# Optimization experiments

Measured on AMD Instinct MI355X. Metric: run time of the kernel, lower is better.

Reference implementation:

```python
import jax, jax.numpy as jnp
import numpy as np

K = 1024
D = 64
BETA = 0.25
EPS = 1e-10


def setup_inputs() -> dict:
    key = jax.random.key(0)
    k1, k2 = jax.random.split(key)
    z = jax.random.normal(k1, (64, D, 32, 32), dtype=jnp.float32)
    # embedding.weight.data.uniform_(-1/K, 1/K)
    emb = jax.random.uniform(k2, (K, D), dtype=jnp.float32,
                             minval=-1.0 / K, maxval=1.0 / K)
    return {"z": z, "emb": emb}


def reference(z, emb):
    sg = jax.lax.stop_gradient
    B, C, H, W = z.shape  # C == D
    zp = jnp.transpose(z, (0, 2, 3, 1))            # [B,H,W,D]
    zf = zp.reshape(-1, C)                          # [N,D]
    # squared-euclidean distances via matmul (cdist expansion)
    d = (jnp.sum(zf ** 2, axis=1, keepdims=True)
         + jnp.sum(emb ** 2, axis=1)
         - 2.0 * jnp.matmul(zf, emb.T))             # [N,K]
    idx = jnp.argmin(d, axis=1)                     # [N] int
    z_q = emb[idx].reshape(zp.shape)                # gather == one-hot matmul
    loss = (jnp.mean((sg(z_q) - zp) ** 2)
            + BETA * jnp.mean((z_q - sg(zp)) ** 2))
    # straight-through estimator
    z_q_st = zp + sg(z_q - zp)
    # codebook usage perplexity
    n = zf.shape[0]
    e_mean = jnp.zeros((K,), dtype=zf.dtype).at[idx].add(1.0) / n
    perplexity = jnp.exp(-jnp.sum(e_mean * jnp.log(e_mean + EPS)))
    z_q_out = jnp.transpose(z_q_st, (0, 3, 1, 2))   # back to [B,D,H,W]
    return (loss, z_q_out, perplexity, idx.reshape(B, H, W))
```

## Files before the change

### kernel.cpp

```cpp
#include <hip/hip_runtime.h>

#define NVEC 65536
#define KC   1024
#define DD   64
#define NTILE 64
#define KW   256
#define KU   32

#define OUT_ZQ   1
#define OUT_PPL  4194305
#define OUT_IDX  4194306

#define WS_KEYS  0
#define WS_HIST  524288
#define WS_SUMSQ 528384
#define WS_SE    528392
#define WS_EMBT  532488

__global__ __launch_bounds__(256) void prep_kernel(const float* __restrict__ emb,
                                                   float* __restrict__ se,
                                                   float* __restrict__ embT) {
    __shared__ float tile[64][65];
    const int tid = threadIdx.x;
    const int k0  = blockIdx.x * 64;

    {
        const int r = tid >> 2, q = tid & 3;
        const float* row = emb + (size_t)(k0 + r) * 64 + q * 16;
        #pragma unroll
        for (int i = 0; i < 4; ++i) {
            float4 v = *(const float4*)(row + i * 4);
            tile[r][q * 16 + i * 4 + 0] = v.x;
            tile[r][q * 16 + i * 4 + 1] = v.y;
            tile[r][q * 16 + i * 4 + 2] = v.z;
            tile[r][q * 16 + i * 4 + 3] = v.w;
        }
    }
    __syncthreads();

    if (tid < 64) {
        float r[8];
        #pragma unroll
        for (int c = 0; c < 64; ++c) {
            float v = tile[tid][c];
            float s = __fmul_rn(v, v);
            if (c < 8) r[c] = s;
            else       r[c & 7] = __fadd_rn(r[c & 7], s);
        }
        se[k0 + tid] = __fadd_rn(
            __fadd_rn(__fadd_rn(r[0], r[1]), __fadd_rn(r[2], r[3])),
            __fadd_rn(__fadd_rn(r[4], r[5]), __fadd_rn(r[6], r[7])));
    }

    const int kl = tid & 63, cg = tid >> 6;
    #pragma unroll
    for (int i = 0; i < 16; ++i) {
        int c = cg * 16 + i;
        embT[(size_t)c * KC + k0 + kl] = tile[kl][c];
    }
}

__global__ __launch_bounds__(256)
void dist_kernel(const float* __restrict__ z,
                 const float* __restrict__ embT,
                 const float* __restrict__ se,
                 unsigned long long* __restrict__ keys) {
    __shared__ float zt[64][64];
    __shared__ float lds_sz[64];
    __shared__ unsigned long long red[64];

    const int tid  = threadIdx.x;
    const int lane = tid & 63;
    const int w    = tid >> 6;
    const int n0   = blockIdx.x * NTILE;
    const int b    = n0 >> 10;
    const int hw0  = n0 & 1023;

    {
        const float* zbase = z + (size_t)b * 65536 + hw0;
        #pragma unroll
        for (int j = 0; j < 4; ++j) {
            int idx = tid + j * 256;
            int c   = idx >> 4;
            int nl4 = (idx & 15) * 4;
            *(float4*)&zt[c][nl4] = *(const float4*)(zbase + (size_t)c * 1024 + nl4);
        }
        if (tid < 64) red[tid] = 0xFFFFFFFFFFFFFFFFULL;
    }
    __syncthreads();

    if (tid < 64) {
        float r[8];
        #pragma unroll
        for (int c = 0; c < 64; ++c) {
            float v = zt[c][tid];
            float s = __fmul_rn(v, v);
            if (c < 8) r[c] = s;
            else       r[c & 7] = __fadd_rn(r[c & 7], s);
        }
        lds_sz[tid] = __fadd_rn(
            __fadd_rn(__fadd_rn(r[0], r[1]), __fadd_rn(r[2], r[3])),
            __fadd_rn(__fadd_rn(r[4], r[5]), __fadd_rn(r[6], r[7])));
    }
    __syncthreads();

    const float szn = lds_sz[lane];
    const int   kb  = __builtin_amdgcn_readfirstlane(w * KW);

    float dbest = 3.4e38f;
    int   kbestv = 0;

    for (int g = 0; g < KW; g += KU) {
        const int kg = kb + g;
        float acc[KU];
        #pragma unroll
        for (int j = 0; j < KU; ++j) acc[j] = 0.0f;

        #pragma unroll 2
        for (int c = 0; c < 64; ++c) {
            const float zc = zt[c][lane];
            const float* __restrict__ eb = embT + (size_t)c * KC + kg;
            #pragma unroll
            for (int j = 0; j < KU; ++j)
                acc[j] = __fmaf_rn(zc, eb[j], acc[j]);
        }

        const float* __restrict__ sb = se + kg;
        #pragma unroll
        for (int j = 0; j < KU; ++j) {
            float d = __fmaf_rn(-2.0f, acc[j], __fadd_rn(szn, sb[j]));
            if (d < dbest) { dbest = d; kbestv = kg + j; }
        }
    }

    unsigned m = __float_as_uint(dbest);
    m ^= ((int)m < 0) ? 0xFFFFFFFFu : 0x80000000u;
    atomicMin(&red[lane], ((unsigned long long)m << 10) | (unsigned)kbestv);
    __syncthreads();
    if (tid < 64) keys[n0 + tid] = red[tid];
}

__global__ __launch_bounds__(256) void epilogue_kernel(const float* __restrict__ z,
                                                       const float* __restrict__ emb,
                                                       const unsigned long long* __restrict__ keys,
                                                       float* __restrict__ out,
                                                       int* __restrict__ hist,
                                                       double* __restrict__ sumsq) {
    __shared__ double red[256];
    const int tid = threadIdx.x;
    const int n   = blockIdx.x * 256 + tid;
    const int b   = n >> 10;
    const int hw  = n & 1023;
    const int idx = (int)(keys[n] & 1023ULL);

    out[OUT_IDX + n] = (float)idx;
    atomicAdd(&hist[idx], 1);

    const float* zp = z   + (size_t)b * 65536 + hw;
    float*       op = out + OUT_ZQ + (size_t)b * 65536 + hw;
    const float* er = emb + (size_t)idx * DD;
    double s = 0.0;
    #pragma unroll
    for (int c = 0; c < DD; ++c) {
        float zv   = zp[(size_t)c * 1024];
        float ev   = er[c];
        float diff = ev - zv;
        op[(size_t)c * 1024] = zv + diff;
        s = fma((double)diff, (double)diff, s);
    }
    red[tid] = s;
    __syncthreads();
    for (int off = 128; off > 0; off >>= 1) {
        if (tid < off) red[tid] += red[tid + off];
        __syncthreads();
    }
    if (tid == 0) atomicAdd(sumsq, red[0]);
}

__global__ __launch_bounds__(256) void final_kernel(const int* __restrict__ hist,
                                                    const double* __restrict__ sumsq,
                                                    float* __restrict__ out) {
    __shared__ double red[256];
    const int tid = threadIdx.x;
    double s = 0.0;
    #pragma unroll
    for (int j = 0; j < 4; ++j) {
        int   kk = j * 256 + tid;
        float em = (float)hist[kk] * (1.0f / 65536.0f);
        float t  = em * logf(em + 1e-10f);
        s += (double)t;
    }
    red[tid] = s;
    __syncthreads();
    for (int off = 128; off > 0; off >>= 1) {
        if (tid < off) red[tid] += red[tid + off];
        __syncthreads();
    }
    if (tid == 0) {
        out[OUT_PPL] = expf(-(float)red[0]);
        out[0]       = 1.25f * (float)(sumsq[0] / 4194304.0);
    }
}

extern "C" void kernel_launch(void* const* d_in, const int* in_sizes, int n_in,
                              void* d_out, int out_size, void* d_ws, size_t ws_size,
                              hipStream_t stream) {
    const float* z   = (const float*)d_in[0];
    const float* emb = (const float*)d_in[1];
    float* out = (float*)d_out;
    char*  ws  = (char*)d_ws;

    unsigned long long* keys  = (unsigned long long*)(ws + WS_KEYS);
    int*                hist  = (int*)(ws + WS_HIST);
    double*             sumsq = (double*)(ws + WS_SUMSQ);
    float*              se    = (float*)(ws + WS_SE);
    float*              embT  = (float*)(ws + WS_EMBT);

    hipMemsetAsync(hist, 0, (size_t)KC * 4 + 8, stream);

    prep_kernel<<<KC / 64, 256, 0, stream>>>(emb, se, embT);
    dist_kernel<<<NVEC / NTILE, 256, 0, stream>>>(z, embT, se, keys);
    epilogue_kernel<<<NVEC / 256, 256, 0, stream>>>(z, emb, keys, out, hist, sumsq);
    final_kernel<<<1, 256, 0, stream>>>(hist, sumsq, out);
}
```

Baseline: 151.7 us.

## Split codebook across grid y, precompute z norms, drop LDS staging

The distance kernel now splits the codebook across two blocks per 64-vector tile (grid y), with each wave covering 128 codes instead of 256. This doubles the block count to improve occupancy and latency hiding. z squared norms move into a separate prep kernel that uses the z_q output region as scratch. z columns are read directly from global memory instead of being staged in LDS. The per-vector argmin reduction now uses global 64-bit atomicMin on a keys buffer pre-filled with 0xFF, which adds a memset and more global atomics and reloads z once per block.

```diff
diff --git a/kernel.cpp b/kernel.cpp
--- a/kernel.cpp
+++ b/kernel.cpp
@@ -4,7 +4,8 @@
 #define KC   1024
 #define DD   64
 #define NTILE 64
-#define KW   256
+#define KSPLIT 2
+#define KW   128
 #define KU   32
 
 #define OUT_ZQ   1
@@ -17,13 +18,30 @@
 #define WS_SE    528392
 #define WS_EMBT  532488
 
-__global__ __launch_bounds__(256) void prep_kernel(const float* __restrict__ emb,
-                                                   float* __restrict__ se,
-                                                   float* __restrict__ embT) {
+__global__ __launch_bounds__(256) void prep_z(const float* __restrict__ z,
+                                              float* __restrict__ sz) {
+    const int n  = blockIdx.x * 256 + threadIdx.x;
+    const int b  = n >> 10;
+    const int hw = n & 1023;
+    const float* zp = z + (size_t)b * 65536 + hw;
+    float r[8];
+    #pragma unroll
+    for (int c = 0; c < 64; ++c) {
+        float v = zp[(size_t)c * 1024];
+        float s = __fmul_rn(v, v);
+        if (c < 8) r[c] = s;
+        else       r[c & 7] = __fadd_rn(r[c & 7], s);
+    }
+    sz[n] = __fadd_rn(__fadd_rn(__fadd_rn(r[0], r[1]), __fadd_rn(r[2], r[3])),
+                      __fadd_rn(__fadd_rn(r[4], r[5]), __fadd_rn(r[6], r[7])));
+}
+
+__global__ __launch_bounds__(256) void prep_emb(const float* __restrict__ emb,
+                                                float* __restrict__ se,
+                                                float* __restrict__ embT) {
     __shared__ float tile[64][65];
     const int tid = threadIdx.x;
     const int k0  = blockIdx.x * 64;
-
     {
         const int r = tid >> 2, q = tid & 3;
         const float* row = emb + (size_t)(k0 + r) * 64 + q * 16;
@@ -37,7 +55,6 @@
         }
     }
     __syncthreads();
-
     if (tid < 64) {
         float r[8];
         #pragma unroll
@@ -51,7 +68,6 @@
             __fadd_rn(__fadd_rn(r[0], r[1]), __fadd_rn(r[2], r[3])),
             __fadd_rn(__fadd_rn(r[4], r[5]), __fadd_rn(r[6], r[7])));
     }
-
     const int kl = tid & 63, cg = tid >> 6;
     #pragma unroll
     for (int i = 0; i < 16; ++i) {
@@ -64,50 +80,22 @@
 void dist_kernel(const float* __restrict__ z,
                  const float* __restrict__ embT,
                  const float* __restrict__ se,
+                 const float* __restrict__ sz,
                  unsigned long long* __restrict__ keys) {
-    __shared__ float zt[64][64];
-    __shared__ float lds_sz[64];
-    __shared__ unsigned long long red[64];
-
     const int tid  = threadIdx.x;
     const int lane = tid & 63;
-    const int w    = tid >> 6;
     const int n0   = blockIdx.x * NTILE;
     const int b    = n0 >> 10;
     const int hw0  = n0 & 1023;
-
-    {
-        const float* zbase = z + (size_t)b * 65536 + hw0;
-        #pragma unroll
-        for (int j = 0; j < 4; ++j) {
-            int idx = tid + j * 256;
-            int c   = idx >> 4;
-            int nl4 = (idx & 15) * 4;
-            *(float4*)&zt[c][nl4] = *(const float4*)(zbase + (size_t)c * 1024 + nl4);
-        }
-        if (tid < 64) red[tid] = 0xFFFFFFFFFFFFFFFFULL;
-    }
-    __syncthreads();
-
-    if (tid < 64) {
-        float r[8];
-        #pragma unroll
-        for (int c = 0; c < 64; ++c) {
-            float v = zt[c][tid];
-            float s = __fmul_rn(v, v);
-            if (c < 8) r[c] = s;
-            else       r[c & 7] = __fadd_rn(r[c & 7], s);
-        }
-        lds_sz[tid] = __fadd_rn(
-            __fadd_rn(__fadd_rn(r[0], r[1]), __fadd_rn(r[2], r[3])),
-            __fadd_rn(__fadd_rn(r[4], r[5]), __fadd_rn(r[6], r[7])));
-    }
-    __syncthreads();
-
-    const float szn = lds_sz[lane];
-    const int   kb  = __builtin_amdgcn_readfirstlane(w * KW);
-
-    float dbest = 3.4e38f;
+    const int n    = n0 + lane;
+
+    const float szn = sz[n];
+    const int   kb  = __builtin_amdgcn_readfirstlane(
+                          (blockIdx.y * 4 + (tid >> 6)) * KW);
+
+    const float* __restrict__ zbase = z + (size_t)b * 65536 + hw0 + lane;
+
+    float dbest  = 3.4e38f;
     int   kbestv = 0;
 
     for (int g = 0; g < KW; g += KU) {
@@ -116,9 +104,9 @@
         #pragma unroll
         for (int j = 0; j < KU; ++j) acc[j] = 0.0f;
 
-        #pragma unroll 2
+        #pragma unroll 4
         for (int c = 0; c < 64; ++c) {
-            const float zc = zt[c][lane];
+            const float zc = zbase[(size_t)c * 1024];
             const float* __restrict__ eb = embT + (size_t)c * KC + kg;
             #pragma unroll
             for (int j = 0; j < KU; ++j)
@@ -135,9 +123,7 @@
 
     unsigned m = __float_as_uint(dbest);
     m ^= ((int)m < 0) ? 0xFFFFFFFFu : 0x80000000u;
-    atomicMin(&red[lane], ((unsigned long long)m << 10) | (unsigned)kbestv);
-    __syncthreads();
-    if (tid < 64) keys[n0 + tid] = red[tid];
+    atomicMin(&keys[n], ((unsigned long long)m << 10) | (unsigned)kbestv);
 }
 
 __global__ __launch_bounds__(256) void epilogue_kernel(const float* __restrict__ z,
@@ -215,11 +201,14 @@
     double*             sumsq = (double*)(ws + WS_SUMSQ);
     float*              se    = (float*)(ws + WS_SE);
     float*              embT  = (float*)(ws + WS_EMBT);
-
+    float*              sz    = out + OUT_ZQ;
+
+    hipMemsetAsync(keys, 0xFF, (size_t)NVEC * 8, stream);
     hipMemsetAsync(hist, 0, (size_t)KC * 4 + 8, stream);
 
-    prep_kernel<<<KC / 64, 256, 0, stream>>>(emb, se, embT);
-    dist_kernel<<<NVEC / NTILE, 256, 0, stream>>>(z, embT, se, keys);
+    prep_z  <<<NVEC / 256, 256, 0, stream>>>(z, sz);
+    prep_emb<<<KC / 64,    256, 0, stream>>>(emb, se, embT);
+    dist_kernel<<<dim3(NVEC / NTILE, KSPLIT), 256, 0, stream>>>(z, embT, se, sz, keys);
     epilogue_kernel<<<NVEC / 256, 256, 0, stream>>>(z, emb, keys, out, hist, sumsq);
     final_kernel<<<1, 256, 0, stream>>>(hist, sumsq, out);
 }
```

Result: slower. 174.8 us (+15.2%).
